# Kernel tuning notes

Measured on AMD Instinct MI355X. Metric: run time of the kernel, lower is better.

Reference implementation:

```python
import jax, jax.numpy as jnp
import numpy as np

NUM_HEADS = 8
SCALE = 1.0
BN_EPS = 1e-5


def _mlp1d(x, W1, g1, b1, W2):
    # Conv1d(k=1, bias=False) -> BatchNorm1d (training-mode batch stats) -> ReLU -> Conv1d(k=1, bias=False)
    h = jnp.einsum('oi,bil->bol', W1, x)
    mu = h.mean(axis=(0, 2), keepdims=True)
    var = h.var(axis=(0, 2), keepdims=True)  # biased var, as torch BN training
    h = (h - mu) * jax.lax.rsqrt(var + BN_EPS)
    h = jax.nn.relu(h * g1[None, :, None] + b1[None, :, None])
    return jnp.einsum('oi,bil->bol', W2, h)


def setup_inputs() -> dict:
    key = jax.random.key(0)
    ks = jax.random.split(key, 8)
    b, c, hh, ww = 64, 2048, 14, 14
    hid, out = 4096, 256
    d = {'x': jax.random.normal(ks[0], (b, c, hh, ww), jnp.float32)}

    def w(k, o, i):
        return jax.random.normal(k, (o, i), jnp.float32) * np.float32(1.0 / np.sqrt(i))

    i = 1
    for pre in ('p', 'pp', 'po'):  # proj, proj_pixel, proj_obj
        d[pre + 'W1'] = w(ks[i], hid, c); i += 1
        d[pre + 'G1'] = jnp.ones((hid,), jnp.float32)
        d[pre + 'B1'] = jnp.zeros((hid,), jnp.float32)
        d[pre + 'W2'] = w(ks[i], out, hid); i += 1
    return d


def reference(x, pW1, pG1, pB1, pW2, ppW1, ppG1, ppB1, ppW2, poW1, poG1, poB1, poW2):
    b, c, h, w = x.shape
    xf = x.reshape(b, c, h * w)                      # flatten(2)
    x_pool = xf.mean(axis=2, keepdims=True)          # adaptive_avg_pool2d(x, 1)
    z_g = _mlp1d(x_pool, pW1, pG1, pB1, pW2)         # [b, 256, 1]
    z_feat = _mlp1d(xf, ppW1, ppG1, ppB1, ppW2)      # [b, 256, hw]
    # F.normalize(dim=1) with eps=1e-12, then /scale
    nrm = jnp.maximum(jnp.linalg.norm(z_feat, axis=1, keepdims=True), 1e-12)
    attn = (z_feat / nrm) / SCALE
    attn = attn.reshape(b, NUM_HEADS, -1, h * w)     # [b, nh, 256/nh, hw]
    attn = jax.nn.softmax(attn, axis=-1)
    x4 = xf.reshape(b, NUM_HEADS, c // NUM_HEADS, h * w)
    # torch.matmul(x, obj_attn.transpose(3, 2)) : [b,nh,c/nh,hw] @ [b,nh,hw,q]
    obj_val = jnp.einsum('bnkl,bnql->bnkq', x4, attn).reshape(b, c, -1)  # [b, c, 256/nh]
    obj_val = _mlp1d(obj_val, poW1, poG1, poB1, poW2)                    # [b, 256, 32]
    return z_g, obj_val
```

## Files before the change

### kernel.cpp

```cpp
#include <hip/hip_runtime.h>
#include <hip/hip_bf16.h>

using bf16 = __hip_bfloat16;
typedef __bf16 bf16x8v __attribute__((ext_vector_type(8)));
typedef float f32x4 __attribute__((ext_vector_type(4)));

#define BN_EPS 1e-5f

__device__ __forceinline__ void stval(float* p, float v) { *p = v; }
__device__ __forceinline__ void stval(bf16* p, float v)  { *p = __float2bfloat16(v); }

__device__ __forceinline__ void gload_lds16(const void* g, void* l) {
    __builtin_amdgcn_global_load_lds(
        (const __attribute__((address_space(1))) unsigned int*)g,
        (__attribute__((address_space(3))) unsigned int*)l,
        16, 0, 0);
}

__device__ __forceinline__ int xcd_swz(int orig, int nwg) {
    int q = nwg >> 3, r = nwg & 7;
    int xcd = orig & 7, idx = orig >> 3;
    return (xcd < r ? xcd * (q + 1) : r * (q + 1) + (xcd - r) * q) + idx;
}

template<typename TC>
__global__ __launch_bounds__(512, 2) void mfma_tn8(
    const bf16* __restrict__ A, const bf16* __restrict__ B, TC* __restrict__ C,
    int M, int N, int K, float* __restrict__ ps, float* __restrict__ pq)
{
    __shared__ alignas(16) char lds[163840];
    const int NT = K >> 6;
    const int tid = threadIdx.x;
    const int lane = tid & 63;
    const int wv = tid >> 6;
    const int wm = wv >> 2;
    const int wn = wv & 3;

    const int nbx = gridDim.x;
    int flat = blockIdx.y * nbx + blockIdx.x;
    const int cpx = (nbx * gridDim.y) >> 3;
    flat = (flat & 7) * cpx + (flat >> 3);
    const int mtile = flat / nbx;
    const long m0 = (long)mtile * 256;
    const long n0 = (long)(flat % nbx) * 256;

    const int trow = tid >> 3;
    const int ks = (((tid & 7) ^ ((tid >> 3) & 7)) << 3);
    const bf16* Arow0 = A + (m0 + trow) * (long)K + ks;
    const bf16* Brow0 = B + (n0 + trow) * (long)K + ks;

    auto stage_a = [&](int abuf, int kt) {
        const bf16* g = Arow0 + ((long)kt << 6);
        char* d = (char*)lds + abuf * 32768 + tid * 16;
        gload_lds16(g, d);
        gload_lds16(g + ((long)K << 6),  d + 8192);
        gload_lds16(g + ((long)K << 7),  d + 16384);
        gload_lds16(g + 192L * (long)K,  d + 24576);
    };
    auto stage_b = [&](int bbuf, int kt) {
        const bf16* g = Brow0 + ((long)kt << 6);
        char* d = (char*)lds + 98304 + bbuf * 32768 + tid * 16;
        gload_lds16(g, d);
        gload_lds16(g + ((long)K << 6),  d + 8192);
        gload_lds16(g + ((long)K << 7),  d + 16384);
        gload_lds16(g + 192L * (long)K,  d + 24576);
    };

    const int fr = lane & 15, fc = lane >> 4;
    const int ca0 = ((fc ^ (fr & 7)) << 4);
    const int ca1 = (((4 + fc) ^ (fr & 7)) << 4);

    f32x4 acc[8][4];
#pragma unroll
    for (int m = 0; m < 8; ++m)
#pragma unroll
        for (int n = 0; n < 4; ++n) acc[m][n] = (f32x4){0.f, 0.f, 0.f, 0.f};

    stage_a(0, 0); stage_b(0, 0); stage_a(1, 1);

    for (int T = 0; T < NT; ++T) {
        const int aT = T % 3, bT = T & 1;

        if (T < NT - 1) { asm volatile("s_waitcnt vmcnt(4)" ::: "memory"); }
        else            { asm volatile("s_waitcnt vmcnt(0)" ::: "memory"); }
        __builtin_amdgcn_s_barrier();
        __builtin_amdgcn_sched_barrier(0);

        if (T + 1 < NT) stage_b((T + 1) & 1, T + 1);
        if (T + 2 < NT) stage_a((T + 2) % 3, T + 2);

        const char* Ard = (const char*)lds + aT * 32768 + (wm * 128 + fr) * 128;
        const char* Brd = (const char*)lds + 98304 + bT * 32768 + (wn * 64 + fr) * 128;

        bf16x8v a0[8], a1[8], bl[4], bh[4];
#pragma unroll
        for (int m = 0; m < 8; ++m) {
            a0[m] = *(const bf16x8v*)(Ard + m * 2048 + ca0);
            a1[m] = *(const bf16x8v*)(Ard + m * 2048 + ca1);
        }
#pragma unroll
        for (int n = 0; n < 4; ++n) {
            bl[n] = *(const bf16x8v*)(Brd + n * 2048 + ca0);
            bh[n] = *(const bf16x8v*)(Brd + n * 2048 + ca1);
        }

        __builtin_amdgcn_s_setprio(1);
#pragma unroll
        for (int m = 0; m < 8; ++m)
#pragma unroll
            for (int n = 0; n < 4; ++n) {
                acc[m][n] = __builtin_amdgcn_mfma_f32_16x16x32_bf16(a0[m], bl[n], acc[m][n], 0, 0, 0);
                acc[m][n] = __builtin_amdgcn_mfma_f32_16x16x32_bf16(a1[m], bh[n], acc[m][n], 0, 0, 0);
            }
        __builtin_amdgcn_s_setprio(0);
    }

#pragma unroll
    for (int m = 0; m < 8; ++m) {
        long gr = m0 + wm * 128 + m * 16 + fc * 4;
#pragma unroll
        for (int n = 0; n < 4; ++n) {
            long gc = n0 + wn * 64 + n * 16 + fr;
            TC* cp = C + gr * N + gc;
#pragma unroll
            for (int r = 0; r < 4; ++r) stval(cp + (long)r * N, acc[m][n][r]);
        }
    }

    if (ps != nullptr) {
        __syncthreads();
        float* red = (float*)lds;
        float cs[4], cq[4];
#pragma unroll
        for (int n = 0; n < 4; ++n) {
            float s = 0.f, q = 0.f;
#pragma unroll
            for (int m = 0; m < 8; ++m)
#pragma unroll
                for (int r = 0; r < 4; ++r) {
                    float v = __bfloat162float(__float2bfloat16(acc[m][n][r]));
                    s += v; q += v * v;
                }
            s += __shfl_xor(s, 16, 64); s += __shfl_xor(s, 32, 64);
            q += __shfl_xor(q, 16, 64); q += __shfl_xor(q, 32, 64);
            cs[n] = s; cq[n] = q;
        }
        if (fc == 0) {
#pragma unroll
            for (int n = 0; n < 4; ++n) {
                red[wv * 64 + n * 16 + fr] = cs[n];
                red[512 + wv * 64 + n * 16 + fr] = cq[n];
            }
        }
        __syncthreads();
        if (tid < 256) {
            int c = tid, wnn = c >> 6, idx = c & 63;
            float s = red[wnn * 64 + idx] + red[(4 + wnn) * 64 + idx];
            float q = red[512 + wnn * 64 + idx] + red[512 + (4 + wnn) * 64 + idx];
            ps[(long)mtile * N + n0 + c] = s;
            pq[(long)mtile * N + n0 + c] = q;
        }
    }
}

template<typename TC>
__global__ __launch_bounds__(256) void mfma_tn(
    const bf16* __restrict__ A, const bf16* __restrict__ B, TC* __restrict__ C,
    int M, int N, int K, float* __restrict__ ps, float* __restrict__ pq)
{
    __shared__ alignas(16) unsigned short As[128 * 32];
    __shared__ alignas(16) unsigned short Bs[128 * 32];

    const int tid = threadIdx.x;
    const int l = tid & 63;
    const int nwg = gridDim.x * gridDim.y;
    int s = xcd_swz(blockIdx.y * gridDim.x + blockIdx.x, nwg);
    const int by = s / gridDim.x, bx = s % gridDim.x;
    const long m0 = (long)by * 128;
    const long n0 = (long)bx * 128;
    const int wr = (tid >> 7) & 1;
    const int wc = (tid >> 6) & 1;

    const int off0 = tid * 16;
    const int row0 = off0 >> 6;
    const int kp0  = (off0 >> 4) & 3;
    const bf16* Ag0 = A + (m0 + row0) * (long)K + kp0 * 8;
    const bf16* Ag1 = A + (m0 + row0 + 64) * (long)K + kp0 * 8;
    const bf16* Bg0 = B + (n0 + row0) * (long)K + kp0 * 8;
    const bf16* Bg1 = B + (n0 + row0 + 64) * (long)K + kp0 * 8;
    char* Asl0 = (char*)As + off0;
    char* Asl1 = (char*)As + off0 + 4096;
    char* Bsl0 = (char*)Bs + off0;
    char* Bsl1 = (char*)Bs + off0 + 4096;

    f32x4 acc[4][4];
#pragma unroll
    for (int m = 0; m < 4; ++m)
#pragma unroll
        for (int n = 0; n < 4; ++n) acc[m][n] = (f32x4){0.f, 0.f, 0.f, 0.f};

    const int fr = l & 15;
    const int fc = l >> 4;
    int aoff[4], boff[4];
#pragma unroll
    for (int m = 0; m < 4; ++m) aoff[m] = ((wr * 64 + m * 16 + fr) * 4 + fc) * 16;
#pragma unroll
    for (int n = 0; n < 4; ++n) boff[n] = ((wc * 64 + n * 16 + fr) * 4 + fc) * 16;

    for (int k0 = 0; k0 < K; k0 += 32) {
        gload_lds16(Ag0 + k0, Asl0);
        gload_lds16(Ag1 + k0, Asl1);
        gload_lds16(Bg0 + k0, Bsl0);
        gload_lds16(Bg1 + k0, Bsl1);
        __syncthreads();

        bf16x8v af[4], bfr[4];
#pragma unroll
        for (int m = 0; m < 4; ++m) af[m]  = *(const bf16x8v*)((const char*)As + aoff[m]);
#pragma unroll
        for (int n = 0; n < 4; ++n) bfr[n] = *(const bf16x8v*)((const char*)Bs + boff[n]);
#pragma unroll
        for (int m = 0; m < 4; ++m)
#pragma unroll
            for (int n = 0; n < 4; ++n)
                acc[m][n] = __builtin_amdgcn_mfma_f32_16x16x32_bf16(af[m], bfr[n], acc[m][n], 0, 0, 0);
        __syncthreads();
    }

#pragma unroll
    for (int m = 0; m < 4; ++m) {
        long gr = m0 + wr * 64 + m * 16 + fc * 4;
#pragma unroll
        for (int n = 0; n < 4; ++n) {
            long gc = n0 + wc * 64 + n * 16 + fr;
            TC* cp = C + gr * N + gc;
#pragma unroll
            for (int r = 0; r < 4; ++r) stval(cp + (long)r * N, acc[m][n][r]);
        }
    }

    if (ps != nullptr) {
        float* red = (float*)As;
        float cs[4], cq[4];
#pragma unroll
        for (int n = 0; n < 4; ++n) {
            float s2 = 0.f, q2 = 0.f;
#pragma unroll
            for (int m = 0; m < 4; ++m)
#pragma unroll
                for (int r = 0; r < 4; ++r) {
                    float v = __bfloat162float(__float2bfloat16(acc[m][n][r]));
                    s2 += v; q2 += v * v;
                }
            s2 += __shfl_xor(s2, 16, 64); s2 += __shfl_xor(s2, 32, 64);
            q2 += __shfl_xor(q2, 16, 64); q2 += __shfl_xor(q2, 32, 64);
            cs[n] = s2; cq[n] = q2;
        }
        if (fc == 0) {
#pragma unroll
            for (int n = 0; n < 4; ++n) {
                int c = wc * 64 + n * 16 + fr;
                red[wr * 128 + c] = cs[n];
                red[256 + wr * 128 + c] = cq[n];
            }
        }
        __syncthreads();
        if (tid < 128) {
            float sv = red[tid] + red[128 + tid];
            float qv = red[256 + tid] + red[384 + tid];
            ps[(long)by * N + n0 + tid] = sv;
            pq[(long)by * N + n0 + tid] = qv;
        }
    }
}

__global__ __launch_bounds__(256) void mfma_tn_skbn(
    const bf16* __restrict__ A, const bf16* __restrict__ B, float* __restrict__ Cp,
    int M, int N, int K, int KCH, const float* __restrict__ ta, const float* __restrict__ tc)
{
    __shared__ alignas(16) unsigned short As[128 * 32];
    __shared__ alignas(16) unsigned short Bs[128 * 32];

    const int tid = threadIdx.x;
    const int l = tid & 63;
    const int gxy = gridDim.x * gridDim.y;
    const int nwg = gxy * gridDim.z;
    int s = xcd_swz((blockIdx.z * gridDim.y + blockIdx.y) * gridDim.x + blockIdx.x, nwg);
    const int bz = s / gxy;
    const int rem = s % gxy;
    const int by = rem / gridDim.x, bx = rem % gridDim.x;
    const long m0 = (long)by * 128;
    const long n0 = (long)bx * 128;
    const int wr = (tid >> 7) & 1;
    const int wc = (tid >> 6) & 1;
    const int ksrt = bz * KCH;

    const int off0 = tid * 16;
    const int row0 = off0 >> 6;
    const int kp0  = (off0 >> 4) & 3;
    const bf16* Ag0 = A + (m0 + row0) * (long)K + kp0 * 8 + ksrt;
    const bf16* Ag1 = A + (m0 + row0 + 64) * (long)K + kp0 * 8 + ksrt;
    const bf16* Bg0 = B + (n0 + row0) * (long)K + kp0 * 8 + ksrt;
    const bf16* Bg1 = B + (n0 + row0 + 64) * (long)K + kp0 * 8 + ksrt;
    char* Asl0 = (char*)As + off0;
    char* Asl1 = (char*)As + off0 + 4096;
    char* Bsl0 = (char*)Bs + off0;
    char* Bsl1 = (char*)Bs + off0 + 4096;

    f32x4 acc[4][4];
#pragma unroll
    for (int m = 0; m < 4; ++m)
#pragma unroll
        for (int n = 0; n < 4; ++n) acc[m][n] = (f32x4){0.f, 0.f, 0.f, 0.f};

    const int fr = l & 15;
    const int fc = l >> 4;
    int aoff[4], boff[4];
#pragma unroll
    for (int m = 0; m < 4; ++m) aoff[m] = ((wr * 64 + m * 16 + fr) * 4 + fc) * 16;
#pragma unroll
    for (int n = 0; n < 4; ++n) boff[n] = ((wc * 64 + n * 16 + fr) * 4 + fc) * 16;

    for (int k0 = 0; k0 < KCH; k0 += 32) {
        gload_lds16(Bg0 + k0, Bsl0);
        gload_lds16(Bg1 + k0, Bsl1);

        union { bf16 h[8]; uint4 u; } r0, r1;
        r0.u = *(const uint4*)(Ag0 + k0);
        r1.u = *(const uint4*)(Ag1 + k0);
        const int kb = ksrt + k0 + kp0 * 8;
        float4 av0 = *(const float4*)(ta + kb);
        float4 av1 = *(const float4*)(ta + kb + 4);
        float4 cv0 = *(const float4*)(tc + kb);
        float4 cv1 = *(const float4*)(tc + kb + 4);
        float av[8] = {av0.x, av0.y, av0.z, av0.w, av1.x, av1.y, av1.z, av1.w};
        float cv[8] = {cv0.x, cv0.y, cv0.z, cv0.w, cv1.x, cv1.y, cv1.z, cv1.w};
#pragma unroll
        for (int j = 0; j < 8; ++j) {
            float v = fmaxf(fmaf(av[j], __bfloat162float(r0.h[j]), cv[j]), 0.f);
            r0.h[j] = __float2bfloat16(v);
            v = fmaxf(fmaf(av[j], __bfloat162float(r1.h[j]), cv[j]), 0.f);
            r1.h[j] = __float2bfloat16(v);
        }
        *(uint4*)Asl0 = r0.u;
        *(uint4*)Asl1 = r1.u;
        __syncthreads();

        bf16x8v af[4], bfr[4];
#pragma unroll
        for (int m = 0; m < 4; ++m) af[m]  = *(const bf16x8v*)((const char*)As + aoff[m]);
#pragma unroll
        for (int n = 0; n < 4; ++n) bfr[n] = *(const bf16x8v*)((const char*)Bs + boff[n]);
#pragma unroll
        for (int m = 0; m < 4; ++m)
#pragma unroll
            for (int n = 0; n < 4; ++n)
                acc[m][n] = __builtin_amdgcn_mfma_f32_16x16x32_bf16(af[m], bfr[n], acc[m][n], 0, 0, 0);
        __syncthreads();
    }

    float* Cb = Cp + (long)bz * M * N;
#pragma unroll
    for (int m = 0; m < 4; ++m) {
        long gr = m0 + wr * 64 + m * 16 + fc * 4;
#pragma unroll
        for (int n = 0; n < 4; ++n) {
            long gc = n0 + wc * 64 + n * 16 + fr;
            float* cp = Cb + gr * N + gc;
#pragma unroll
            for (int r = 0; r < 4; ++r) cp[(long)r * N] = acc[m][n][r];
        }
    }
}

__global__ __launch_bounds__(256) void objmm_k(
    const bf16* __restrict__ attnP, const bf16* __restrict__ xP, bf16* __restrict__ objinT)
{
    __shared__ alignas(16) unsigned short As[32 * 32];
    __shared__ alignas(16) unsigned short Bs[256 * 32];
    const int tid = threadIdx.x, lane = tid & 63, wv = tid >> 6;
    const int b = blockIdx.x >> 3, h = blockIdx.x & 7;
    const bf16* Ab = attnP + ((long)(b * 256 + h * 32)) * 224;
    const bf16* Bb = xP + ((long)(b * 2048 + h * 256)) * 224;
    const int fr = lane & 15, fc = lane >> 4;
    const int srow = tid >> 2, schk = tid & 3;

    f32x4 acc[2][4];
#pragma unroll
    for (int m = 0; m < 2; ++m)
#pragma unroll
        for (int n = 0; n < 4; ++n) acc[m][n] = (f32x4){0.f, 0.f, 0.f, 0.f};

    for (int k0 = 0; k0 < 224; k0 += 32) {
        if (wv < 2)
            gload_lds16(Ab + (long)srow * 224 + schk * 8 + k0, (char*)As + tid * 16);
#pragma unroll
        for (int j = 0; j < 4; ++j)
            gload_lds16(Bb + (long)(j * 64 + srow) * 224 + schk * 8 + k0,
                        (char*)Bs + j * 4096 + tid * 16);
        __syncthreads();

        bf16x8v af[2], bfr[4];
#pragma unroll
        for (int m = 0; m < 2; ++m)
            af[m] = *(const bf16x8v*)((const char*)As + (m * 16 + fr) * 64 + fc * 16);
#pragma unroll
        for (int n = 0; n < 4; ++n)
            bfr[n] = *(const bf16x8v*)((const char*)Bs + (wv * 64 + n * 16 + fr) * 64 + fc * 16);
#pragma unroll
        for (int m = 0; m < 2; ++m)
#pragma unroll
            for (int n = 0; n < 4; ++n)
                acc[m][n] = __builtin_amdgcn_mfma_f32_16x16x32_bf16(af[m], bfr[n], acc[m][n], 0, 0, 0);
        __syncthreads();
    }

#pragma unroll
    for (int m = 0; m < 2; ++m) {
        long gr = (long)b * 32 + m * 16 + fc * 4;
#pragma unroll
        for (int n = 0; n < 4; ++n) {
            long gc = (long)h * 256 + wv * 64 + n * 16 + fr;
            bf16* cp = objinT + gr * 2048 + gc;
#pragma unroll
            for (int r = 0; r < 4; ++r) cp[(long)r * 2048] = __float2bfloat16(acc[m][n][r]);
        }
    }
}

__global__ __launch_bounds__(256) void foldnorm_k(const float* __restrict__ p,
    float* __restrict__ z, float* __restrict__ invn)
{
    int j = blockIdx.x * 4 + (threadIdx.x >> 6);
    int lane = threadIdx.x & 63;
    float4 a = *(const float4*)(p + (long)j * 256 + lane * 4);
    float4 b = *(const float4*)(p + 3211264L + (long)j * 256 + lane * 4);
    float4 s; s.x = a.x + b.x; s.y = a.y + b.y; s.z = a.z + b.z; s.w = a.w + b.w;
    *(float4*)(z + (long)j * 256 + lane * 4) = s;
    float q = s.x * s.x + s.y * s.y + s.z * s.z + s.w * s.w;
#pragma unroll
    for (int off = 32; off; off >>= 1) q += __shfl_xor(q, off, 64);
    if (lane == 0) invn[j] = 1.f / fmaxf(sqrtf(q), 1e-12f);
}

__global__ __launch_bounds__(256) void foldout_k(const float* __restrict__ p, float* __restrict__ out)
{
    int o = blockIdx.x * 256 + threadIdx.x;
    int b = o >> 13, rem = o & 8191, q = rem >> 5, tt = rem & 31;
    long base = ((long)(b * 32 + tt)) * 256 + q;
    float s = p[base] + p[524288 + base] + p[2 * 524288 + base] + p[3 * 524288 + base];
    out[o] = s;
}

__global__ __launch_bounds__(256) void convert4_k(
    const float* __restrict__ w1, const float* __restrict__ w2,
    const float* __restrict__ w3, const float* __restrict__ w4,
    bf16* __restrict__ o1, bf16* __restrict__ o2,
    bf16* __restrict__ o3, bf16* __restrict__ o4)
{
    const long L1 = 8388608, L2 = 1048576;
    long i = ((long)blockIdx.x * 256 + threadIdx.x) * 8;
    const float* src; bf16* dst; long e;
    if (i < L1)                { src = w1; dst = o1; e = i; }
    else if (i < L1 + L2)      { src = w2; dst = o2; e = i - L1; }
    else if (i < 2*L1 + L2)    { src = w3; dst = o3; e = i - L1 - L2; }
    else if (i < 2*L1 + 2*L2)  { src = w4; dst = o4; e = i - 2*L1 - L2; }
    else return;
    float4 v0 = *(const float4*)(src + e);
    float4 v1 = *(const float4*)(src + e + 4);
    union { bf16 h[8]; uint4 u; } r;
    r.h[0] = __float2bfloat16(v0.x); r.h[1] = __float2bfloat16(v0.y);
    r.h[2] = __float2bfloat16(v0.z); r.h[3] = __float2bfloat16(v0.w);
    r.h[4] = __float2bfloat16(v1.x); r.h[5] = __float2bfloat16(v1.y);
    r.h[6] = __float2bfloat16(v1.z); r.h[7] = __float2bfloat16(v1.w);
    *(uint4*)(dst + e) = r.u;
}

__global__ __launch_bounds__(256) void packx2_k(const float* __restrict__ x,
    bf16* __restrict__ XT, bf16* __restrict__ xP, float* __restrict__ xpT)
{
    __shared__ unsigned short tile[196 * 66 + 4];
    __shared__ float pp[64];
    const int t = threadIdx.x;
    const int b = blockIdx.y, c0 = blockIdx.x * 64;
    const int wvi = t >> 6, lane = t & 63;

    for (int p = 0; p < 16; ++p) {
        int c = p * 4 + wvi;
        const float* row = x + ((long)b * 2048 + c0 + c) * 196;
        float v0 = row[lane];
        float v1 = row[lane + 64];
        float v2 = row[lane + 128];
        float v3 = (lane < 4) ? row[lane + 192] : 0.f;
        bf16 h0 = __float2bfloat16(v0);
        bf16 h1 = __float2bfloat16(v1);
        bf16 h2 = __float2bfloat16(v2);
        bf16 h3 = __float2bfloat16(v3);
        tile[lane * 66 + c]         = *(unsigned short*)&h0;
        tile[(lane + 64) * 66 + c]  = *(unsigned short*)&h1;
        tile[(lane + 128) * 66 + c] = *(unsigned short*)&h2;
        if (lane < 4) tile[(lane + 192) * 66 + c] = *(unsigned short*)&h3;
        float s = v0 + v1 + v2 + v3;
#pragma unroll
        for (int off = 32; off; off >>= 1) s += __shfl_xor(s, off, 64);
        if (lane == 0) pp[c] = s;
    }
    __syncthreads();
    if (t < 64) xpT[(c0 + t) * 64 + b] = pp[t] * (1.f / 196.f);

    for (int u = t; u < 196 * 8; u += 256) {
        int l = u >> 3, cc = u & 7;
        const unsigned short* sp = &tile[l * 66 + cc * 8];
        uint4 r;
        r.x = *(const unsigned int*)(sp);
        r.y = *(const unsigned int*)(sp + 2);
        r.z = *(const unsigned int*)(sp + 4);
        r.w = *(const unsigned int*)(sp + 6);
        *(uint4*)(&XT[((long)b * 196 + l) * 2048 + c0 + cc * 8]) = r;
    }

    for (int u = t; u < 64 * 28; u += 256) {
        int c = u / 28, ch = u % 28;
        int l0 = ch * 8;
        union { unsigned short h[8]; uint4 v; } r;
#pragma unroll
        for (int e = 0; e < 8; ++e) {
            int ll = l0 + e;
            r.h[e] = (ll < 196) ? tile[ll * 66 + c] : (unsigned short)0;
        }
        *(uint4*)(xP + ((long)b * 2048 + c0 + c) * 224 + l0) = r.v;
    }
}

__global__ __launch_bounds__(256) void colstat2_k(const float* __restrict__ ps, const float* __restrict__ pq,
    int P, float invN, const float* __restrict__ g, const float* __restrict__ be,
    float* __restrict__ ta, float* __restrict__ tc)
{
    int c = blockIdx.x * 256 + threadIdx.x;
    float s = 0.f, q = 0.f;
    for (int p = 0; p < P; ++p) { s += ps[(long)p * 4096 + c]; q += pq[(long)p * 4096 + c]; }
    float mu  = s * invN;
    float var = q * invN - mu * mu;
    float a   = g[c] * rsqrtf(var + BN_EPS);
    ta[c] = a;
    tc[c] = be[c] - mu * a;
}

__global__ __launch_bounds__(256) void softmax2_k(const float* __restrict__ z,
    const float* __restrict__ invn, bf16* __restrict__ attnP)
{
    int row  = blockIdx.x * 4 + (threadIdx.x >> 6);
    int lane = threadIdx.x & 63;
    int b = row >> 8, q = row & 255;
    float v[4];
    float mx = -INFINITY;
#pragma unroll
    for (int i = 0; i < 4; ++i) {
        int l = lane + 64 * i;
        if (l < 196) {
            int j = b * 196 + l;
            v[i] = z[(long)j * 256 + q] * invn[j];
        } else v[i] = -INFINITY;
        mx = fmaxf(mx, v[i]);
    }
#pragma unroll
    for (int off = 32; off; off >>= 1) mx = fmaxf(mx, __shfl_xor(mx, off, 64));
    float s = 0.f;
#pragma unroll
    for (int i = 0; i < 4; ++i) {
        v[i] = (lane + 64 * i < 196) ? __expf(v[i] - mx) : 0.f;
        s += v[i];
    }
#pragma unroll
    for (int off = 32; off; off >>= 1) s += __shfl_xor(s, off, 64);
    float is = 1.f / s;
    bf16* rp = attnP + (long)row * 224;
#pragma unroll
    for (int i = 0; i < 4; ++i) {
        int l = lane + 64 * i;
        if (l < 196) rp[l] = __float2bfloat16(v[i] * is);
        else if (l < 224) rp[l] = __float2bfloat16(0.f);
    }
}

template<bool TRANS>
__global__ __launch_bounds__(256) void gemmsk_k(
    const float* __restrict__ A, const float* __restrict__ B, float* __restrict__ Cp,
    int M, int N, int K, int lda, int ldbk, int KCH,
    const float* __restrict__ tra, const float* __restrict__ trc)
{
    constexpr int BM = 64, BN = 64, BK = 16;
    __shared__ float As[BK][BM + 4];
    __shared__ float Bs[BK][BN + 4];

    const int tid = threadIdx.x;
    const int m0 = blockIdx.y * BM;
    const int ks = blockIdx.z * KCH;
    const int ke = min(K, ks + KCH);

    const int tIdm = tid / 16;
    const int tIdn = tid % 16;
    const int aK  = tid % BK;
    const int aM0 = tid / BK;
    const int bN  = tid % BN;
    const int bK0 = tid / BN;

    float acc[4][4];
#pragma unroll
    for (int u = 0; u < 4; ++u)
#pragma unroll
        for (int v = 0; v < 4; ++v) acc[u][v] = 0.f;

    for (int k0 = ks; k0 < ke; k0 += BK) {
#pragma unroll
        for (int i = 0; i < 4; ++i) {
            int m = aM0 + 16 * i;
            int gk = k0 + aK, gm = m0 + m;
            float v = 0.f;
            if (gk < ke && gm < M) v = A[(long)gm * lda + gk];
            As[aK][m] = v;
        }
#pragma unroll
        for (int i = 0; i < 4; ++i) {
            int kk = bK0 + 4 * i;
            int gk = k0 + kk;
            float v = 0.f;
            if (gk < ke && bN < N) {
                v = B[(long)gk * ldbk + bN];
                if (TRANS) v = fmaxf(tra[gk] * v + trc[gk], 0.f);
            }
            Bs[kk][bN] = v;
        }
        __syncthreads();
#pragma unroll
        for (int kk = 0; kk < BK; ++kk) {
            float a[4], b[4];
#pragma unroll
            for (int u = 0; u < 4; ++u) a[u] = As[kk][tIdm * 4 + u];
#pragma unroll
            for (int v = 0; v < 4; ++v) b[v] = Bs[kk][tIdn * 4 + v];
#pragma unroll
            for (int u = 0; u < 4; ++u)
#pragma unroll
                for (int v = 0; v < 4; ++v)
                    acc[u][v] = fmaf(a[u], b[v], acc[u][v]);
        }
        __syncthreads();
    }

    float* Cb = Cp + (long)blockIdx.z * M * N;
#pragma unroll
    for (int u = 0; u < 4; ++u) {
        int gm = m0 + tIdm * 4 + u;
        if (gm >= M) continue;
#pragma unroll
        for (int v = 0; v < 4; ++v) {
            int gn = tIdn * 4 + v;
            if (gn < N) Cb[(long)gm * N + gn] = acc[u][v];
        }
    }
}

__global__ __launch_bounds__(256) void skbn_k(const float* __restrict__ Cp,
    const float* __restrict__ g, const float* __restrict__ be,
    float* __restrict__ h1, float* __restrict__ ta, float* __restrict__ tc)
{
    int o = blockIdx.x * 4 + (threadIdx.x >> 6);
    int b = threadIdx.x & 63;
    float s = 0.f;
#pragma unroll
    for (int p = 0; p < 16; ++p) s += Cp[(long)p * 262144 + o * 64 + b];
    h1[o * 64 + b] = s;
    float s1 = s, s2 = s * s;
#pragma unroll
    for (int off = 32; off; off >>= 1) {
        s1 += __shfl_down(s1, off, 64);
        s2 += __shfl_down(s2, off, 64);
    }
    if (b == 0) {
        float mu  = s1 * (1.f / 64.f);
        float var = s2 * (1.f / 64.f) - mu * mu;
        float a   = g[o] * rsqrtf(var + BN_EPS);
        ta[o] = a;
        tc[o] = be[o] - mu * a;
    }
}

__global__ __launch_bounds__(256) void skreduce_k(const float* __restrict__ Cp, int P, long MN,
    int Nn, int ldm, int ldn, float* __restrict__ out)
{
    long i = (long)blockIdx.x * 256 + threadIdx.x;
    if (i >= MN) return;
    float s = 0.f;
    for (int p = 0; p < P; ++p) s += Cp[(long)p * MN + i];
    int m = (int)(i / Nn), n = (int)(i % Nn);
    out[(long)m * ldm + (long)n * ldn] = s;
}

extern "C" void kernel_launch(void* const* d_in, const int* in_sizes, int n_in,
                              void* d_out, int out_size, void* d_ws, size_t ws_size,
                              hipStream_t stream)
{
    const float* x    = (const float*)d_in[0];
    const float* pW1  = (const float*)d_in[1];
    const float* pG1  = (const float*)d_in[2];
    const float* pB1  = (const float*)d_in[3];
    const float* pW2  = (const float*)d_in[4];
    const float* ppW1 = (const float*)d_in[5];
    const float* ppG1 = (const float*)d_in[6];
    const float* ppB1 = (const float*)d_in[7];
    const float* ppW2 = (const float*)d_in[8];
    const float* poW1 = (const float*)d_in[9];
    const float* poG1 = (const float*)d_in[10];
    const float* poB1 = (const float*)d_in[11];
    const float* poW2 = (const float*)d_in[12];
    float* out = (float*)d_out;
    (void)in_sizes; (void)n_in; (void)out_size; (void)ws_size;

    char* w = (char*)d_ws;
    auto alloc = [&](size_t bytes) -> char* {
        char* p = w; w += (bytes + 255) & ~(size_t)255; return p;
    };
    bf16* ppW1b = (bf16*)alloc((size_t)4096 * 2048 * 2);
    bf16* ppW2b = (bf16*)alloc((size_t)256 * 4096 * 2);
    bf16* poW1b = (bf16*)alloc((size_t)4096 * 2048 * 2);
    bf16* poW2b = (bf16*)alloc((size_t)256 * 4096 * 2);
    char* region1 = alloc((size_t)12544 * 2048 * 2);
    bf16*  XT     = (bf16*)region1;
    bf16*  attnP  = (bf16*)region1;
    bf16*  objinT = (bf16*)(region1 + 12845056);
    bf16*  hobjT  = (bf16*)(region1 + 12845056 + 8388608);
    bf16* xP     = (bf16*)alloc((size_t)64 * 2048 * 224 * 2);
    bf16* hfeatT = (bf16*)alloc((size_t)12544 * 4096 * 2);
    float* zfeatT = (float*)alloc((size_t)12544 * 256 * 4);
    float* ps    = (float*)alloc((size_t)49 * 4096 * 4);
    float* pq    = (float*)alloc((size_t)49 * 4096 * 4);
    float* invn  = (float*)alloc((size_t)12544 * 4);
    float* a2    = (float*)alloc(4096 * 4);
    float* c2    = (float*)alloc(4096 * 4);
    float* a3    = (float*)alloc(4096 * 4);
    float* c3    = (float*)alloc(4096 * 4);
    float* xpT   = (float*)alloc((size_t)2048 * 64 * 4);
    float* h1    = (float*)alloc((size_t)4096 * 64 * 4);
    float* a1    = (float*)alloc(4096 * 4);
    float* c1    = (float*)alloc(4096 * 4);
    float* skp1  = (float*)alloc((size_t)16 * 4096 * 64 * 4);
    float* skp2  = (float*)alloc((size_t)32 * 256 * 64 * 4);
    float* skp5  = (float*)alloc((size_t)4 * 2048 * 256 * 4);
    float* skpG2 = (float*)alloc((size_t)2 * 12544 * 256 * 4);

    convert4_k<<<9216, 256, 0, stream>>>(ppW1, ppW2, poW1, poW2, ppW1b, ppW2b, poW1b, poW2b);
    packx2_k<<<dim3(32, 64), 256, 0, stream>>>(x, XT, xP, xpT);

    gemmsk_k<false><<<dim3(1, 64, 16), 256, 0, stream>>>(
        pW1, xpT, skp1, 4096, 64, 2048, 2048, 64, 128, nullptr, nullptr);
    skbn_k<<<1024, 256, 0, stream>>>(skp1, pG1, pB1, h1, a1, c1);
    gemmsk_k<true><<<dim3(1, 4, 32), 256, 0, stream>>>(
        pW2, h1, skp2, 256, 64, 4096, 4096, 64, 128, a1, c1);
    skreduce_k<<<64, 256, 0, stream>>>(skp2, 32, (long)256 * 64, 64, 1, 256, out);

    mfma_tn8<bf16><<<dim3(16, 49), 512, 0, stream>>>(XT, ppW1b, hfeatT, 12544, 4096, 2048, ps, pq);
    colstat2_k<<<16, 256, 0, stream>>>(ps, pq, 49, 1.f / 12544.f, ppG1, ppB1, a2, c2);

    mfma_tn_skbn<<<dim3(2, 98, 2), 256, 0, stream>>>(
        hfeatT, ppW2b, skpG2, 12544, 256, 4096, 2048, a2, c2);
    foldnorm_k<<<3136, 256, 0, stream>>>(skpG2, zfeatT, invn);

    softmax2_k<<<4096, 256, 0, stream>>>(zfeatT, invn, attnP);

    objmm_k<<<512, 256, 0, stream>>>(attnP, xP, objinT);

    mfma_tn<bf16><<<dim3(32, 16), 256, 0, stream>>>(objinT, poW1b, hobjT, 2048, 4096, 2048, ps, pq);
    colstat2_k<<<16, 256, 0, stream>>>(ps, pq, 16, 1.f / 2048.f, poG1, poB1, a3, c3);

    mfma_tn_skbn<<<dim3(2, 16, 4), 256, 0, stream>>>(
        hobjT, poW2b, skp5, 2048, 256, 4096, 1024, a3, c3);
    foldout_k<<<2048, 256, 0, stream>>>(skp5, out + 16384);
}
```

Before: 639.3 us.

## Restructure big GEMM LDS pipeline to double-buffer with split B phases; raise split-K

After: 613.0 us. -4.1%, faster.

```diff
diff --git a/kernel.cpp b/kernel.cpp
--- a/kernel.cpp
+++ b/kernel.cpp
@@ -28,7 +28,7 @@
     const bf16* __restrict__ A, const bf16* __restrict__ B, TC* __restrict__ C,
     int M, int N, int K, float* __restrict__ ps, float* __restrict__ pq)
 {
-    __shared__ alignas(16) char lds[163840];
+    __shared__ char lds[131072];
     const int NT = K >> 6;
     const int tid = threadIdx.x;
     const int lane = tid & 63;
@@ -48,10 +48,12 @@
     const int ks = (((tid & 7) ^ ((tid >> 3) & 7)) << 3);
     const bf16* Arow0 = A + (m0 + trow) * (long)K + ks;
     const bf16* Brow0 = B + (n0 + trow) * (long)K + ks;
-
-    auto stage_a = [&](int abuf, int kt) {
+    char* ldsA = (char*)lds + tid * 16;
+    char* ldsB = (char*)lds + 32768 + tid * 16;
+
+    auto stage_a = [&](int bbuf, int kt) {
         const bf16* g = Arow0 + ((long)kt << 6);
-        char* d = (char*)lds + abuf * 32768 + tid * 16;
+        char* d = ldsA + (bbuf << 16);
         gload_lds16(g, d);
         gload_lds16(g + ((long)K << 6),  d + 8192);
         gload_lds16(g + ((long)K << 7),  d + 16384);
@@ -59,7 +61,7 @@
     };
     auto stage_b = [&](int bbuf, int kt) {
         const bf16* g = Brow0 + ((long)kt << 6);
-        char* d = (char*)lds + 98304 + bbuf * 32768 + tid * 16;
+        char* d = ldsB + (bbuf << 16);
         gload_lds16(g, d);
         gload_lds16(g + ((long)K << 6),  d + 8192);
         gload_lds16(g + ((long)K << 7),  d + 16384);
@@ -76,42 +78,60 @@
 #pragma unroll
         for (int n = 0; n < 4; ++n) acc[m][n] = (f32x4){0.f, 0.f, 0.f, 0.f};
 
-    stage_a(0, 0); stage_b(0, 0); stage_a(1, 1);
+    stage_a(0, 0); stage_b(0, 0); stage_a(1, 1); stage_b(1, 1);
 
     for (int T = 0; T < NT; ++T) {
-        const int aT = T % 3, bT = T & 1;
-
-        if (T < NT - 1) { asm volatile("s_waitcnt vmcnt(4)" ::: "memory"); }
-        else            { asm volatile("s_waitcnt vmcnt(0)" ::: "memory"); }
+        const int bb = T & 1;
+        const char* Ard = (const char*)lds + (bb << 16) + (wm * 128 + fr) * 128;
+        const char* Brd = (const char*)lds + (bb << 16) + 32768 + (wn * 64 + fr) * 128;
+
+        if (T == 0)          { asm volatile("s_waitcnt vmcnt(8)" ::: "memory"); }
+        else if (T < NT - 1) { asm volatile("s_waitcnt vmcnt(4)" ::: "memory"); }
+        else                 { asm volatile("s_waitcnt vmcnt(0)" ::: "memory"); }
         __builtin_amdgcn_s_barrier();
         __builtin_amdgcn_sched_barrier(0);
 
-        if (T + 1 < NT) stage_b((T + 1) & 1, T + 1);
-        if (T + 2 < NT) stage_a((T + 2) % 3, T + 2);
-
-        const char* Ard = (const char*)lds + aT * 32768 + (wm * 128 + fr) * 128;
-        const char* Brd = (const char*)lds + 98304 + bT * 32768 + (wn * 64 + fr) * 128;
-
-        bf16x8v a0[8], a1[8], bl[4], bh[4];
+        bf16x8v a0[8], a1[8];
 #pragma unroll
         for (int m = 0; m < 8; ++m) {
             a0[m] = *(const bf16x8v*)(Ard + m * 2048 + ca0);
             a1[m] = *(const bf16x8v*)(Ard + m * 2048 + ca1);
         }
-#pragma unroll
-        for (int n = 0; n < 4; ++n) {
-            bl[n] = *(const bf16x8v*)(Brd + n * 2048 + ca0);
-            bh[n] = *(const bf16x8v*)(Brd + n * 2048 + ca1);
-        }
+        bf16x8v b00 = *(const bf16x8v*)(Brd + ca0);
+        bf16x8v b01 = *(const bf16x8v*)(Brd + ca1);
+        bf16x8v b10 = *(const bf16x8v*)(Brd + 2048 + ca0);
+        bf16x8v b11 = *(const bf16x8v*)(Brd + 2048 + ca1);
+
+        if (T >= 1 && T + 1 < NT) stage_b(bb ^ 1, T + 1);
 
         __builtin_amdgcn_s_setprio(1);
 #pragma unroll
-        for (int m = 0; m < 8; ++m)
-#pragma unroll
-            for (int n = 0; n < 4; ++n) {
-                acc[m][n] = __builtin_amdgcn_mfma_f32_16x16x32_bf16(a0[m], bl[n], acc[m][n], 0, 0, 0);
-                acc[m][n] = __builtin_amdgcn_mfma_f32_16x16x32_bf16(a1[m], bh[n], acc[m][n], 0, 0, 0);
-            }
+        for (int m = 0; m < 8; ++m) {
+            acc[m][0] = __builtin_amdgcn_mfma_f32_16x16x32_bf16(a0[m], b00, acc[m][0], 0, 0, 0);
+            acc[m][0] = __builtin_amdgcn_mfma_f32_16x16x32_bf16(a1[m], b01, acc[m][0], 0, 0, 0);
+            acc[m][1] = __builtin_amdgcn_mfma_f32_16x16x32_bf16(a0[m], b10, acc[m][1], 0, 0, 0);
+            acc[m][1] = __builtin_amdgcn_mfma_f32_16x16x32_bf16(a1[m], b11, acc[m][1], 0, 0, 0);
+        }
+        __builtin_amdgcn_s_setprio(0);
+
+        __builtin_amdgcn_s_barrier();
+        __builtin_amdgcn_sched_barrier(0);
+
+        bf16x8v b20 = *(const bf16x8v*)(Brd + 2 * 2048 + ca0);
+        bf16x8v b21 = *(const bf16x8v*)(Brd + 2 * 2048 + ca1);
+        bf16x8v b30 = *(const bf16x8v*)(Brd + 3 * 2048 + ca0);
+        bf16x8v b31 = *(const bf16x8v*)(Brd + 3 * 2048 + ca1);
+
+        if (T + 2 < NT) stage_a(bb, T + 2);
+
+        __builtin_amdgcn_s_setprio(1);
+#pragma unroll
+        for (int m = 0; m < 8; ++m) {
+            acc[m][2] = __builtin_amdgcn_mfma_f32_16x16x32_bf16(a0[m], b20, acc[m][2], 0, 0, 0);
+            acc[m][2] = __builtin_amdgcn_mfma_f32_16x16x32_bf16(a1[m], b21, acc[m][2], 0, 0, 0);
+            acc[m][3] = __builtin_amdgcn_mfma_f32_16x16x32_bf16(a0[m], b30, acc[m][3], 0, 0, 0);
+            acc[m][3] = __builtin_amdgcn_mfma_f32_16x16x32_bf16(a1[m], b31, acc[m][3], 0, 0, 0);
+        }
         __builtin_amdgcn_s_setprio(0);
     }
 
@@ -433,13 +453,20 @@
 {
     int j = blockIdx.x * 4 + (threadIdx.x >> 6);
     int lane = threadIdx.x & 63;
-    float4 a = *(const float4*)(p + (long)j * 256 + lane * 4);
-    float4 b = *(const float4*)(p + 3211264L + (long)j * 256 + lane * 4);
-    float4 s; s.x = a.x + b.x; s.y = a.y + b.y; s.z = a.z + b.z; s.w = a.w + b.w;
-    *(float4*)(z + (long)j * 256 + lane * 4) = s;
+    long off = (long)j * 256 + lane * 4;
+    float4 a = *(const float4*)(p + off);
+    float4 b = *(const float4*)(p + 3211264L + off);
+    float4 c = *(const float4*)(p + 2 * 3211264L + off);
+    float4 d = *(const float4*)(p + 3 * 3211264L + off);
+    float4 s;
+    s.x = (a.x + b.x) + (c.x + d.x);
+    s.y = (a.y + b.y) + (c.y + d.y);
+    s.z = (a.z + b.z) + (c.z + d.z);
+    s.w = (a.w + b.w) + (c.w + d.w);
+    *(float4*)(z + off) = s;
     float q = s.x * s.x + s.y * s.y + s.z * s.z + s.w * s.w;
 #pragma unroll
-    for (int off = 32; off; off >>= 1) q += __shfl_xor(q, off, 64);
+    for (int off2 = 32; off2; off2 >>= 1) q += __shfl_xor(q, off2, 64);
     if (lane == 0) invn[j] = 1.f / fmaxf(sqrtf(q), 1e-12f);
 }
 
@@ -448,7 +475,9 @@
     int o = blockIdx.x * 256 + threadIdx.x;
     int b = o >> 13, rem = o & 8191, q = rem >> 5, tt = rem & 31;
     long base = ((long)(b * 32 + tt)) * 256 + q;
-    float s = p[base] + p[524288 + base] + p[2 * 524288 + base] + p[3 * 524288 + base];
+    float s = 0.f;
+#pragma unroll
+    for (int z = 0; z < 8; ++z) s += p[(long)z * 524288 + base];
     out[o] = s;
 }
 
@@ -727,6 +756,7 @@
     bf16* poW2b = (bf16*)alloc((size_t)256 * 4096 * 2);
     char* region1 = alloc((size_t)12544 * 2048 * 2);
     bf16*  XT     = (bf16*)region1;
+    float* skpG2  = (float*)region1;
     bf16*  attnP  = (bf16*)region1;
     bf16*  objinT = (bf16*)(region1 + 12845056);
     bf16*  hobjT  = (bf16*)(region1 + 12845056 + 8388608);
@@ -746,8 +776,7 @@
     float* c1    = (float*)alloc(4096 * 4);
     float* skp1  = (float*)alloc((size_t)16 * 4096 * 64 * 4);
     float* skp2  = (float*)alloc((size_t)32 * 256 * 64 * 4);
-    float* skp5  = (float*)alloc((size_t)4 * 2048 * 256 * 4);
-    float* skpG2 = (float*)alloc((size_t)2 * 12544 * 256 * 4);
+    float* skp5  = (float*)alloc((size_t)8 * 2048 * 256 * 4);
 
     convert4_k<<<9216, 256, 0, stream>>>(ppW1, ppW2, poW1, poW2, ppW1b, ppW2b, poW1b, poW2b);
     packx2_k<<<dim3(32, 64), 256, 0, stream>>>(x, XT, xP, xpT);
@@ -762,8 +791,8 @@
     mfma_tn8<bf16><<<dim3(16, 49), 512, 0, stream>>>(XT, ppW1b, hfeatT, 12544, 4096, 2048, ps, pq);
     colstat2_k<<<16, 256, 0, stream>>>(ps, pq, 49, 1.f / 12544.f, ppG1, ppB1, a2, c2);
 
-    mfma_tn_skbn<<<dim3(2, 98, 2), 256, 0, stream>>>(
-        hfeatT, ppW2b, skpG2, 12544, 256, 4096, 2048, a2, c2);
+    mfma_tn_skbn<<<dim3(2, 98, 4), 256, 0, stream>>>(
+        hfeatT, ppW2b, skpG2, 12544, 256, 4096, 1024, a2, c2);
     foldnorm_k<<<3136, 256, 0, stream>>>(skpG2, zfeatT, invn);
 
     softmax2_k<<<4096, 256, 0, stream>>>(zfeatT, invn, attnP);
@@ -773,7 +802,7 @@
     mfma_tn<bf16><<<dim3(32, 16), 256, 0, stream>>>(objinT, poW1b, hobjT, 2048, 4096, 2048, ps, pq);
     colstat2_k<<<16, 256, 0, stream>>>(ps, pq, 16, 1.f / 2048.f, poG1, poB1, a3, c3);
 
-    mfma_tn_skbn<<<dim3(2, 16, 4), 256, 0, stream>>>(
-        hobjT, poW2b, skp5, 2048, 256, 4096, 1024, a3, c3);
+    mfma_tn_skbn<<<dim3(2, 16, 8), 256, 0, stream>>>(
+        hobjT, poW2b, skp5, 2048, 256, 4096, 512, a3, c3);
     foldout_k<<<2048, 256, 0, stream>>>(skp5, out + 16384);
 }
```
